# Kernel optimization log

Hardware: AMD Instinct MI355X
Metric: run time of the kernel (lower is better)

Reference implementation:

```python
import jax, jax.numpy as jnp
import numpy as np

N_USERS = 100000
N_ITEMS = 50000
N_NODES = N_USERS + N_ITEMS
D = 64
N_LAYERS = 3
POP_BINS = 10
NNZ = 2000000
BATCH = 256
BIAS_SCALE = 1.0


def setup_inputs() -> dict:
    key = jax.random.key(0)
    ks = jax.random.split(key, 16)
    std = 0.01
    inp = {
        "user_emb": jax.random.normal(ks[0], (N_USERS, D), jnp.float32) * std,
        "item_emb": jax.random.normal(ks[1], (N_ITEMS, D), jnp.float32) * std,
        "user_bias": jnp.zeros((N_USERS, 1), jnp.float32),
        "item_bias": jnp.zeros((N_ITEMS, 1), jnp.float32),
        "pop_emb": jax.random.normal(ks[2], (POP_BINS, D), jnp.float32) * std,
        "uW1": jax.random.normal(ks[3], (D, D), jnp.float32) / np.sqrt(D),
        "ub1": jnp.zeros((D,), jnp.float32),
        "uW2": jax.random.normal(ks[4], (D, D), jnp.float32) / np.sqrt(D),
        "ub2": jnp.zeros((D,), jnp.float32),
        "iW1": jax.random.normal(ks[5], (D, D), jnp.float32) / np.sqrt(D),
        "ib1": jnp.zeros((D,), jnp.float32),
        "iW2": jax.random.normal(ks[6], (D, D), jnp.float32) / np.sqrt(D),
        "ib2": jnp.zeros((D,), jnp.float32),
        "gW1": jax.random.normal(ks[7], (2 * D, D), jnp.float32) / np.sqrt(2 * D),
        "gb1": jnp.zeros((D,), jnp.float32),
        "gW2": jax.random.normal(ks[8], (D, 1), jnp.float32) / np.sqrt(D),
        "gb2": jnp.zeros((1,), jnp.float32),
        "adj_vals": jax.random.uniform(ks[9], (NNZ,), jnp.float32),
        "adj_rows": jax.random.randint(ks[10], (NNZ,), 0, N_NODES, jnp.int32),
        "adj_cols": jax.random.randint(ks[11], (NNZ,), 0, N_NODES, jnp.int32),
        "item_pop_bins": jax.random.randint(ks[12], (N_ITEMS,), 0, POP_BINS, jnp.int32),
        "users": jax.random.randint(ks[13], (BATCH,), 0, N_USERS, jnp.int32),
    }
    return inp


def _spmm(vals, rows, cols, E):
    # sparse (N x N) @ E  via gather + segment-sum
    msgs = vals[:, None] * E[cols]          # [nnz, d]
    return jax.ops.segment_sum(msgs, rows, num_segments=N_NODES)


def _mlp2(x, W1, b1, W2, b2):
    return jax.nn.relu(x @ W1 + b1) @ W2 + b2


def reference(user_emb, item_emb, user_bias, item_bias, pop_emb,
              uW1, ub1, uW2, ub2, iW1, ib1, iW2, ib2,
              gW1, gb1, gW2, gb2,
              adj_vals, adj_rows, adj_cols, item_pop_bins, users):
    # ---- computer(): LightGCN propagation with uniform layer weights ----
    emb = jnp.concatenate([user_emb, item_emb], axis=0)   # [N, d]
    w = 1.0 / (N_LAYERS + 1)
    out = emb * w
    cur = emb
    for _ in range(N_LAYERS):
        cur = _spmm(adj_vals, adj_rows, adj_cols, cur)
        out = out + cur * w
    all_users, all_items = out[:N_USERS], out[N_USERS:]

    # ---- popularity-gated item fusion ----
    p_vec = pop_emb[item_pop_bins]                         # [n_items, d]
    gate_in = jnp.concatenate([all_items, p_vec], axis=-1)
    z = jax.nn.sigmoid(_mlp2(gate_in, gW1, gb1, gW2, gb2)) # [n_items, 1]
    items_fused = (1.0 - z) * all_items + z * p_vec

    # ---- two-tower scoring over all items ----
    U = _mlp2(all_users[users], uW1, ub1, uW2, ub2)        # [B, d]
    I = _mlp2(items_fused, iW1, ib1, iW2, ib2)             # [n_items, d]
    scores = U @ I.T                                        # [B, n_items]
    scores = scores + user_bias[users] * BIAS_SCALE + (item_bias.T) * BIAS_SCALE
    return scores
```

## Files before the change

### kernel.cpp

```cpp
#include <hip/hip_runtime.h>
#include <hip/hip_fp16.h>

#define N_USERS 100000
#define N_ITEMS 50000
#define N_NODES 150000
#define D 64
#define NNZ 2000000
#define BATCH 256
#define POP_BINS 10

#define BSH 9
#define NB2 293
#define CAP 8192
#define P1_EPB 2048
#define P1_BLOCKS 978

#define ST_P 130

__global__ __launch_bounds__(256) void k_prep(const float* __restrict__ ue,
                                              const float* __restrict__ ie,
                                              __half* __restrict__ Eh,
                                              const float* __restrict__ pop,
                                              const float* __restrict__ gW1,
                                              const float* __restrict__ iW1,
                                              float* __restrict__ hp,
                                              float* __restrict__ pp1) {
  int b = blockIdx.x;
  if (b == 9375) {
    for (int idx = threadIdx.x; idx < 2 * POP_BINS * 64; idx += 256) {
      int q = idx;
      bool second = q >= POP_BINS * 64;
      if (second) q -= POP_BINS * 64;
      int bb = q >> 6, o = q & 63;
      float s = 0.f;
      if (!second) {
        for (int k = 0; k < 64; k++) s += pop[bb * 64 + k] * gW1[(64 + k) * 64 + o];
        hp[q] = s;
      } else {
        for (int k = 0; k < 64; k++) s += pop[bb * 64 + k] * iW1[k * 64 + o];
        pp1[q] = s;
      }
    }
    return;
  }
  int t = b * 256 + threadIdx.x;
  size_t fo = (size_t)t * 4;
  const float* src = (fo < (size_t)N_USERS * 64) ? ue + fo
                                                 : ie + (fo - (size_t)N_USERS * 64);
  float4 v = *(const float4*)src;
  __half2* dst = (__half2*)(Eh + fo);
  dst[0] = __floats2half2_rn(v.x, v.y);
  dst[1] = __floats2half2_rn(v.z, v.w);
}

__global__ __launch_bounds__(256) void k_p1(const int* __restrict__ rows,
                                            const int* __restrict__ cols,
                                            const float* __restrict__ vals,
                                            int* __restrict__ bcur,
                                            uint2* __restrict__ gstage) {
  __shared__ int cnt[NB2];
  __shared__ int gbase[NB2];
  int t = threadIdx.x;
  for (int i = t; i < NB2; i += 256) cnt[i] = 0;
  __syncthreads();
  int base = blockIdx.x * P1_EPB;
  for (int i = 0; i < 8; i++) {
    int e = base + i * 256 + t;
    if (e < NNZ) atomicAdd(&cnt[rows[e] >> BSH], 1);
  }
  __syncthreads();
  for (int i = t; i < NB2; i += 256) {
    int c = cnt[i];
    gbase[i] = c ? atomicAdd(&bcur[i], c) : 0;
    cnt[i] = 0;
  }
  __syncthreads();
  for (int i = 0; i < 8; i++) {
    int e = base + i * 256 + t;
    if (e < NNZ) {
      int r = rows[e];
      int b = r >> BSH;
      int rank = atomicAdd(&cnt[b], 1);
      unsigned key = ((unsigned)(r & 511) << 18) | (unsigned)cols[e];
      gstage[(size_t)b * CAP + gbase[b] + rank] =
          make_uint2(key, __float_as_uint(vals[e]));
    }
  }
}

__global__ __launch_bounds__(512) void k_p2(const int* __restrict__ bcur,
                                            const uint2* __restrict__ gstage,
                                            uint2* __restrict__ epack,
                                            int* __restrict__ rowbeg,
                                            int* __restrict__ rowend,
                                            int* __restrict__ gcursor,
                                            const int* __restrict__ users,
                                            int* __restrict__ uflag,
                                            int* __restrict__ ulist,
                                            int* __restrict__ ucnt) {
  int b = blockIdx.x, t = threadIdx.x;
  if (b == NB2) {
    if (t < BATCH) {
      int u = users[t];
      int old = atomicOr(&uflag[u >> 5], 1 << (u & 31));
      if (!((old >> (u & 31)) & 1)) {
        int p = atomicAdd(ucnt, 1);
        ulist[p] = u;
      }
    }
    return;
  }
  __shared__ int cnt[512];
  __shared__ int off[512];
  __shared__ int s[512];
  __shared__ int gbs;
  __shared__ uint2 buf[CAP];
  int n = bcur[b];
  const uint2* gs = gstage + (size_t)b * CAP;
  if (t == 0) gbs = atomicAdd(gcursor, n);
  cnt[t] = 0;
  __syncthreads();
  for (int j = t; j < n; j += 512)
    atomicAdd(&cnt[gs[j].x >> 18], 1);
  __syncthreads();
  int v = cnt[t];
  s[t] = v;
  __syncthreads();
  for (int o = 1; o < 512; o <<= 1) {
    int x = (t >= o) ? s[t - o] : 0;
    __syncthreads();
    s[t] += x;
    __syncthreads();
  }
  int ex = s[t] - v;
  off[t] = ex;
  int base = gbs;
  int gr = (b << BSH) + t;
  if (gr < N_NODES) { rowbeg[gr] = base + ex; rowend[gr] = base + ex + v; }
  __syncthreads();
  for (int j = t; j < n; j += 512) {
    uint2 ed = gs[j];
    int lr = ed.x >> 18;
    int pos = atomicAdd(&off[lr], 1);
    buf[pos] = make_uint2(ed.x & 0x3FFFFu, ed.y);
  }
  __syncthreads();
  for (int j = t; j < n; j += 512) epack[base + j] = buf[j];
}

#define SPMM_QW_BODY(TBL)                                                     \
  float a0 = 0.f, a1 = 0.f, a2 = 0.f, a3 = 0.f;                               \
  int j = beg;                                                                \
  for (; j + 7 < end; j += 8) {                                               \
    uint2 ea = epack[j + q];                                                  \
    uint2 eb = epack[j + 4 + q];                                              \
    uint2 ra = *(const uint2*)(TBL + (size_t)ea.x * 64 + 4 * p);              \
    uint2 rb = *(const uint2*)(TBL + (size_t)eb.x * 64 + 4 * p);              \
    float va = __uint_as_float(ea.y), vb = __uint_as_float(eb.y);             \
    float2 la = __half22float2(*(const __half2*)&ra.x);                       \
    float2 ha = __half22float2(*(const __half2*)&ra.y);                       \
    float2 lb = __half22float2(*(const __half2*)&rb.x);                       \
    float2 hb = __half22float2(*(const __half2*)&rb.y);                       \
    a0 += va * la.x; a1 += va * la.y; a2 += va * ha.x; a3 += va * ha.y;       \
    a0 += vb * lb.x; a1 += vb * lb.y; a2 += vb * hb.x; a3 += vb * hb.y;       \
  }                                                                           \
  for (; j < end; j += 4) {                                                   \
    int jj = j + q;                                                           \
    int jc = (jj < end) ? jj : end - 1;                                       \
    uint2 e = epack[jc];                                                      \
    float v = (jj < end) ? __uint_as_float(e.y) : 0.f;                        \
    uint2 r = *(const uint2*)(TBL + (size_t)e.x * 64 + 4 * p);                \
    float2 lo = __half22float2(*(const __half2*)&r.x);                        \
    float2 hi = __half22float2(*(const __half2*)&r.y);                        \
    a0 += v * lo.x; a1 += v * lo.y; a2 += v * hi.x; a3 += v * hi.y;           \
  }                                                                           \
  a0 += __shfl_xor(a0, 16, 64); a0 += __shfl_xor(a0, 32, 64);                 \
  a1 += __shfl_xor(a1, 16, 64); a1 += __shfl_xor(a1, 32, 64);                 \
  a2 += __shfl_xor(a2, 16, 64); a2 += __shfl_xor(a2, 32, 64);                 \
  a3 += __shfl_xor(a3, 16, 64); a3 += __shfl_xor(a3, 32, 64);

__global__ __launch_bounds__(256) void k_spmm1(const int* __restrict__ rowbeg,
                                               const int* __restrict__ rowend,
                                               const uint2* __restrict__ epack,
                                               const float* __restrict__ ue,
                                               const float* __restrict__ ie,
                                               const __half* __restrict__ Eh0,
                                               const int* __restrict__ uflag,
                                               __half* __restrict__ EoutH,
                                               float* __restrict__ Oacc) {
  int wave = blockIdx.x * 4 + (threadIdx.x >> 6);
  int row = __builtin_amdgcn_readfirstlane(wave);
  if (row >= N_NODES) return;
  int lane = threadIdx.x & 63;
  int p = lane & 15, q = lane >> 4;
  int beg = rowbeg[row];
  int end = rowend[row];
  SPMM_QW_BODY(Eh0)
  if (q == 0) {
    __half2* eo = (__half2*)(EoutH + (size_t)row * 64 + 4 * p);
    eo[0] = __floats2half2_rn(a0, a1);
    eo[1] = __floats2half2_rn(a2, a3);
    bool need = (row >= N_USERS) || (((uflag[row >> 5] >> (row & 31)) & 1) != 0);
    if (need) {
      const float* srow = (row < N_USERS) ? ue + (size_t)row * 64
                                          : ie + (size_t)(row - N_USERS) * 64;
      float4 sv = *(const float4*)(srow + 4 * p);
      *(float4*)(Oacc + (size_t)row * 64 + 4 * p) =
          make_float4(0.25f * (sv.x + a0), 0.25f * (sv.y + a1),
                      0.25f * (sv.z + a2), 0.25f * (sv.w + a3));
    }
  }
}

__global__ __launch_bounds__(256) void k_spmm2h(const int* __restrict__ rowbeg,
                                                const int* __restrict__ rowend,
                                                const uint2* __restrict__ epack,
                                                const __half* __restrict__ Ein,
                                                const int* __restrict__ uflag,
                                                __half* __restrict__ EoutH,
                                                float* __restrict__ Oacc) {
  int wave = blockIdx.x * 4 + (threadIdx.x >> 6);
  int row = __builtin_amdgcn_readfirstlane(wave);
  if (row >= N_NODES) return;
  int lane = threadIdx.x & 63;
  int p = lane & 15, q = lane >> 4;
  int beg = rowbeg[row];
  int end = rowend[row];
  SPMM_QW_BODY(Ein)
  if (q == 0) {
    __half2* eo = (__half2*)(EoutH + (size_t)row * 64 + 4 * p);
    eo[0] = __floats2half2_rn(a0, a1);
    eo[1] = __floats2half2_rn(a2, a3);
    if (row >= N_USERS || (((uflag[row >> 5] >> (row & 31)) & 1) != 0)) {
      float4* op = (float4*)(Oacc + (size_t)row * 64 + 4 * p);
      float4 cur = *op;
      *op = make_float4(cur.x + 0.25f * a0, cur.y + 0.25f * a1,
                        cur.z + 0.25f * a2, cur.w + 0.25f * a3);
    }
  }
}

__global__ __launch_bounds__(256) void k_spmm3h(const int* __restrict__ rowbeg,
                                                const int* __restrict__ rowend,
                                                const uint2* __restrict__ epack,
                                                const __half* __restrict__ Ein,
                                                const int* __restrict__ ulist,
                                                const int* __restrict__ ucnt,
                                                float* __restrict__ Oacc) {
  int w = blockIdx.x * 4 + (threadIdx.x >> 6);
  int row;
  if (w < N_ITEMS) {
    row = N_USERS + w;
  } else {
    int k = w - N_ITEMS;
    if (k >= ucnt[0]) return;
    row = ulist[k];
  }
  row = __builtin_amdgcn_readfirstlane(row);
  int lane = threadIdx.x & 63;
  int p = lane & 15, q = lane >> 4;
  int beg = rowbeg[row];
  int end = rowend[row];
  SPMM_QW_BODY(Ein)
  if (q == 0) {
    float4* op = (float4*)(Oacc + (size_t)row * 64 + 4 * p);
    float4 cur = *op;
    *op = make_float4(cur.x + 0.25f * a0, cur.y + 0.25f * a1,
                      cur.z + 0.25f * a2, cur.w + 0.25f * a3);
  }
}

__global__ __launch_bounds__(256) void k_user(const float* __restrict__ Oacc,
                                              const int* __restrict__ users,
                                              const float* __restrict__ ubias,
                                              const float* __restrict__ uW1,
                                              const float* __restrict__ ub1,
                                              const float* __restrict__ uW2,
                                              const float* __restrict__ ub2,
                                              float* __restrict__ Ut) {
  int ub = blockIdx.x * 4 + (threadIdx.x >> 6);
  int lane = threadIdx.x & 63;
  int u = users[ub];
  float x = Oacc[(size_t)u * 64 + lane];
  float h = ub1[lane];
#pragma unroll
  for (int k = 0; k < 64; k++)
    h = fmaf(__shfl(x, k, 64), uW1[k * 64 + lane], h);
  h = h > 0.f ? h : 0.f;
  float o = ub2[lane];
#pragma unroll
  for (int k = 0; k < 64; k++)
    o = fmaf(__shfl(h, k, 64), uW2[k * 64 + lane], o);
  Ut[lane * 256 + ub] = o;
  if (lane == 0) Ut[64 * 256 + ub] = ubias[u];
}

__global__ __launch_bounds__(256) void k_gemm12(const float* __restrict__ Oacc,
                                                const float* __restrict__ gW1,
                                                const float* __restrict__ iW1,
                                                const int* __restrict__ bins,
                                                const float* __restrict__ hp,
                                                const float* __restrict__ pp1,
                                                const float* __restrict__ gb1,
                                                const float* __restrict__ gW2,
                                                const float* __restrict__ gb2,
                                                const float* __restrict__ ib1,
                                                const float* __restrict__ iW2,
                                                const float* __restrict__ ib2,
                                                float* __restrict__ I) {
  __shared__ float Is[64 * ST_P];
  __shared__ float Bs[64 * 128];
  __shared__ float zp[128][9];
  __shared__ float zs[128];
  int tid = threadIdx.x;
  int i0 = blockIdx.x * 128;
  {
    int c4 = tid & 15, r0 = tid >> 4;
#pragma unroll
    for (int s = 0; s < 8; s++) {
      int r = r0 + s * 16;
      int it = i0 + r;
      float4 v = make_float4(0.f, 0.f, 0.f, 0.f);
      if (it < N_ITEMS) v = *(const float4*)(Oacc + (size_t)(N_USERS + it) * 64 + c4 * 4);
      Is[(c4 * 4 + 0) * ST_P + r] = v.x;
      Is[(c4 * 4 + 1) * ST_P + r] = v.y;
      Is[(c4 * 4 + 2) * ST_P + r] = v.z;
      Is[(c4 * 4 + 3) * ST_P + r] = v.w;
    }
  }
  for (int idx = tid; idx < 64 * 128; idx += 256) {
    int k = idx >> 7, o = idx & 127;
    Bs[idx] = (o < 64) ? gW1[k * 64 + o] : iW1[k * 64 + (o - 64)];
  }
  __syncthreads();
  int tx = tid & 15, ty = tid >> 4;
  float acc[8][8];
#pragma unroll
  for (int a = 0; a < 8; a++)
#pragma unroll
    for (int b = 0; b < 8; b++) acc[a][b] = 0.f;
  {
    const float* ip = Is + tx * 8;
    const float* wp = Bs + ty * 8;
#pragma unroll 2
    for (int k = 0; k < 64; k++) {
      float4 iv0 = *(const float4*)(ip + k * ST_P);
      float4 iv1 = *(const float4*)(ip + k * ST_P + 4);
      float4 wv0 = *(const float4*)(wp + k * 128);
      float4 wv1 = *(const float4*)(wp + k * 128 + 4);
      float iv[8] = {iv0.x, iv0.y, iv0.z, iv0.w, iv1.x, iv1.y, iv1.z, iv1.w};
      float wv[8] = {wv0.x, wv0.y, wv0.z, wv0.w, wv1.x, wv1.y, wv1.z, wv1.w};
#pragma unroll
      for (int a = 0; a < 8; a++)
#pragma unroll
        for (int b = 0; b < 8; b++) acc[a][b] += iv[a] * wv[b];
    }
  }
  int ibase = i0 + tx * 8;
  if (ty < 8) {
    int o0 = ty * 8;
#pragma unroll
    for (int a = 0; a < 8; a++) {
      int it = ibase + a;
      float p = 0.f;
      if (it < N_ITEMS) {
        int bin = bins[it];
        const float* hpr = hp + bin * 64 + o0;
#pragma unroll
        for (int b = 0; b < 8; b++) {
          float g = acc[a][b] + hpr[b] + gb1[o0 + b];
          g = g > 0.f ? g : 0.f;
          p += g * gW2[o0 + b];
        }
      }
      zp[tx * 8 + a][ty] = p;
    }
  }
  __syncthreads();
  if (tid < 128) {
    float s = gb2[0];
#pragma unroll
    for (int k = 0; k < 8; k++) s += zp[tid][k];
    zs[tid] = 1.f / (1.f + expf(-s));
  }
  __syncthreads();
  if (ty >= 8) {
    int o0 = (ty - 8) * 8;
#pragma unroll
    for (int a = 0; a < 8; a++) {
      int it = ibase + a;
      int item = tx * 8 + a;
      float z = zs[item];
      int bin = (it < N_ITEMS) ? bins[it] : 0;
      const float* ppr = pp1 + bin * 64 + o0;
#pragma unroll
      for (int b = 0; b < 8; b++) {
        float v = (1.f - z) * acc[a][b] + z * ppr[b] + ib1[o0 + b];
        Is[(o0 + b) * ST_P + item] = v > 0.f ? v : 0.f;
      }
    }
  }
  for (int idx = tid; idx < 64 * 64; idx += 256) Bs[idx] = iW2[idx];
  __syncthreads();
  float acc2[8][4];
#pragma unroll
  for (int a = 0; a < 8; a++)
#pragma unroll
    for (int b = 0; b < 4; b++) acc2[a][b] = 0.f;
  {
    const float* ip = Is + tx * 8;
    const float* wp = Bs + ty * 4;
#pragma unroll 2
    for (int k = 0; k < 64; k++) {
      float4 iv0 = *(const float4*)(ip + k * ST_P);
      float4 iv1 = *(const float4*)(ip + k * ST_P + 4);
      float4 wv = *(const float4*)(wp + k * 64);
      float iv[8] = {iv0.x, iv0.y, iv0.z, iv0.w, iv1.x, iv1.y, iv1.z, iv1.w};
      float wvv[4] = {wv.x, wv.y, wv.z, wv.w};
#pragma unroll
      for (int a = 0; a < 8; a++)
#pragma unroll
        for (int b = 0; b < 4; b++) acc2[a][b] += iv[a] * wvv[b];
    }
  }
  int oc = ty * 4;
  float b0 = ib2[oc], b1 = ib2[oc + 1], b2 = ib2[oc + 2], b3 = ib2[oc + 3];
#pragma unroll
  for (int a = 0; a < 8; a++) {
    int it = ibase + a;
    if (it < N_ITEMS) {
      float4 s0 = make_float4(acc2[a][0] + b0, acc2[a][1] + b1,
                              acc2[a][2] + b2, acc2[a][3] + b3);
      *(float4*)(I + (size_t)it * 64 + oc) = s0;
    }
  }
}

__global__ __launch_bounds__(256) void k_scores(const float* __restrict__ I,
                                                const float* __restrict__ Ut,
                                                const float* __restrict__ item_bias,
                                                float* __restrict__ out) {
  __shared__ float Is[64 * ST_P];
  __shared__ float Us[64 * 128];
  int tid = threadIdx.x;
  int i0 = blockIdx.x * 128;
  {
    int c4 = tid & 15, r0 = tid >> 4;
#pragma unroll
    for (int s = 0; s < 8; s++) {
      int r = r0 + s * 16;
      int it = i0 + r;
      float4 v = make_float4(0.f, 0.f, 0.f, 0.f);
      if (it < N_ITEMS) v = *(const float4*)(I + (size_t)it * 64 + c4 * 4);
      Is[(c4 * 4 + 0) * ST_P + r] = v.x;
      Is[(c4 * 4 + 1) * ST_P + r] = v.y;
      Is[(c4 * 4 + 2) * ST_P + r] = v.z;
      Is[(c4 * 4 + 3) * ST_P + r] = v.w;
    }
  }
  int tx = tid & 15;
  int ty = tid >> 4;
  int ibase = i0 + tx * 8;
  float ib[8];
#pragma unroll
  for (int a = 0; a < 8; a++)
    ib[a] = (ibase + a < N_ITEMS) ? item_bias[ibase + a] : 0.f;
  for (int uh = 0; uh < 2; uh++) {
    int ubase = uh * 128;
    if (uh) __syncthreads();
    {
      int u4 = tid & 31, k0 = tid >> 5;
#pragma unroll
      for (int s = 0; s < 8; s++) {
        int k = k0 + s * 8;
        float4 v = *(const float4*)(Ut + k * 256 + ubase + u4 * 4);
        *(float4*)(Us + k * 128 + u4 * 4) = v;
      }
    }
    __syncthreads();
    float acc[8][8];
#pragma unroll
    for (int a = 0; a < 8; a++)
#pragma unroll
      for (int b = 0; b < 8; b++) acc[a][b] = 0.f;
    const float* ip = Is + tx * 8;
    const float* up = Us + ty * 8;
#pragma unroll 2
    for (int k = 0; k < 64; k++) {
      float4 iv0 = *(const float4*)(ip + k * ST_P);
      float4 iv1 = *(const float4*)(ip + k * ST_P + 4);
      float4 uv0 = *(const float4*)(up + k * 128);
      float4 uv1 = *(const float4*)(up + k * 128 + 4);
      float iv[8] = {iv0.x, iv0.y, iv0.z, iv0.w, iv1.x, iv1.y, iv1.z, iv1.w};
      float uv[8] = {uv0.x, uv0.y, uv0.z, uv0.w, uv1.x, uv1.y, uv1.z, uv1.w};
#pragma unroll
      for (int a = 0; a < 8; a++)
#pragma unroll
        for (int b = 0; b < 8; b++) acc[a][b] += iv[a] * uv[b];
    }
#pragma unroll
    for (int bb = 0; bb < 8; bb++) {
      int bu = ubase + ty * 8 + bb;
      float ubias = Ut[64 * 256 + bu];
      float* orow = out + (size_t)bu * N_ITEMS + ibase;
      if (ibase + 7 < N_ITEMS) {
        float4 s0 = make_float4(acc[0][bb] + ubias + ib[0], acc[1][bb] + ubias + ib[1],
                                acc[2][bb] + ubias + ib[2], acc[3][bb] + ubias + ib[3]);
        float4 s1 = make_float4(acc[4][bb] + ubias + ib[4], acc[5][bb] + ubias + ib[5],
                                acc[6][bb] + ubias + ib[6], acc[7][bb] + ubias + ib[7]);
        *(float4*)orow = s0;
        *(float4*)(orow + 4) = s1;
      } else {
#pragma unroll
        for (int a = 0; a < 8; a++)
          if (ibase + a < N_ITEMS) orow[a] = acc[a][bb] + ubias + ib[a];
      }
    }
  }
}

extern "C" void kernel_launch(void* const* d_in, const int* in_sizes, int n_in,
                              void* d_out, int out_size, void* d_ws, size_t ws_size,
                              hipStream_t stream) {
  const float* user_emb  = (const float*)d_in[0];
  const float* item_emb  = (const float*)d_in[1];
  const float* user_bias = (const float*)d_in[2];
  const float* item_bias = (const float*)d_in[3];
  const float* pop_emb   = (const float*)d_in[4];
  const float* uW1 = (const float*)d_in[5];
  const float* ub1 = (const float*)d_in[6];
  const float* uW2 = (const float*)d_in[7];
  const float* ub2 = (const float*)d_in[8];
  const float* iW1 = (const float*)d_in[9];
  const float* ib1 = (const float*)d_in[10];
  const float* iW2 = (const float*)d_in[11];
  const float* ib2 = (const float*)d_in[12];
  const float* gW1 = (const float*)d_in[13];
  const float* gb1 = (const float*)d_in[14];
  const float* gW2 = (const float*)d_in[15];
  const float* gb2 = (const float*)d_in[16];
  const float* adj_vals = (const float*)d_in[17];
  const int* adj_rows = (const int*)d_in[18];
  const int* adj_cols = (const int*)d_in[19];
  const int* bins  = (const int*)d_in[20];
  const int* users = (const int*)d_in[21];
  float* out = (float*)d_out;

  float* ws = (float*)d_ws;
  float* Oacc = ws;
  float* bufA = ws + 9600000;
  float* bufB = ws + 19200000;
  uint2* epack = (uint2*)(ws + 28800000);
  int* rowbeg = (int*)(ws + 32800000);
  int* rowend = (int*)(ws + 32950000);
  int* uflag   = (int*)(ws + 33100000);
  int* ucnt    = (int*)(ws + 33103125);
  int* bcur    = (int*)(ws + 33103126);
  int* gcursor = (int*)(ws + 33103419);
  int* ulist   = (int*)(ws + 33103420);
  float* Ut   = ws + 33104000;
  float* hp   = ws + 33121000;
  float* pp1  = ws + 33122000;
  uint2* gstage = (uint2*)bufB;
  __half* Eh0 = (__half*)bufA;
  __half* E1h = (__half*)(bufA + 4800000);
  __half* E2h = (__half*)bufB;
  float* I  = bufB;

  hipMemsetAsync(uflag, 0, 3680 * sizeof(int), stream);
  k_prep<<<9376, 256, 0, stream>>>(user_emb, item_emb, Eh0, pop_emb, gW1, iW1, hp, pp1);
  k_p1<<<P1_BLOCKS, 256, 0, stream>>>(adj_rows, adj_cols, adj_vals, bcur, gstage);
  k_p2<<<NB2 + 1, 512, 0, stream>>>(bcur, gstage, epack, rowbeg, rowend, gcursor,
                                    users, uflag, ulist, ucnt);

  k_spmm1<<<37500, 256, 0, stream>>>(rowbeg, rowend, epack, user_emb, item_emb,
                                     Eh0, uflag, E1h, Oacc);
  k_spmm2h<<<37500, 256, 0, stream>>>(rowbeg, rowend, epack, E1h, uflag, E2h, Oacc);
  k_spmm3h<<<12564, 256, 0, stream>>>(rowbeg, rowend, epack, E2h, ulist, ucnt, Oacc);

  k_user<<<64, 256, 0, stream>>>(Oacc, users, user_bias, uW1, ub1, uW2, ub2, Ut);
  k_gemm12<<<391, 256, 0, stream>>>(Oacc, gW1, iW1, bins, hp, pp1, gb1, gW2, gb2,
                                    ib1, iW2, ib2, I);
  k_scores<<<391, 256, 0, stream>>>(I, Ut, item_bias, out);
}
```

Measured before the change: 486.2 us.

## Replace two-pass bucketed CSR build with histogram, wave-scan claim, and atomic scatter

Replaces the bucketed two-phase COO-to-CSR conversion (shared-memory staging into 293 buckets, then a per-bucket local sort) with three simple kernels. A global per-row atomic histogram is followed by a wavefront-scan kernel that claims contiguous ranges via a global cursor, and then an atomic-cursor scatter writes edges directly into epack. This removes the staging buffer round trip and the per-bucket shared-memory sort, at the cost of 2M global atomics on random rows twice. Row order in memory is no longer row-sorted globally, and edge order within a row becomes nondeterministic.

```diff
diff --git a/kernel.cpp b/kernel.cpp
--- a/kernel.cpp
+++ b/kernel.cpp
@@ -9,11 +9,9 @@
 #define BATCH 256
 #define POP_BINS 10
 
-#define BSH 9
-#define NB2 293
-#define CAP 8192
-#define P1_EPB 2048
-#define P1_BLOCKS 978
+#define H_EPB 2048
+#define H_BLOCKS 978
+#define CLAIM_BLOCKS 587
 
 #define ST_P 130
 
@@ -53,53 +51,26 @@
   dst[1] = __floats2half2_rn(v.z, v.w);
 }
 
-__global__ __launch_bounds__(256) void k_p1(const int* __restrict__ rows,
-                                            const int* __restrict__ cols,
-                                            const float* __restrict__ vals,
-                                            int* __restrict__ bcur,
-                                            uint2* __restrict__ gstage) {
-  __shared__ int cnt[NB2];
-  __shared__ int gbase[NB2];
+__global__ __launch_bounds__(256) void k_hist(const int* __restrict__ rows,
+                                              int* __restrict__ rtmp) {
+  int base = blockIdx.x * H_EPB;
   int t = threadIdx.x;
-  for (int i = t; i < NB2; i += 256) cnt[i] = 0;
-  __syncthreads();
-  int base = blockIdx.x * P1_EPB;
   for (int i = 0; i < 8; i++) {
     int e = base + i * 256 + t;
-    if (e < NNZ) atomicAdd(&cnt[rows[e] >> BSH], 1);
-  }
-  __syncthreads();
-  for (int i = t; i < NB2; i += 256) {
-    int c = cnt[i];
-    gbase[i] = c ? atomicAdd(&bcur[i], c) : 0;
-    cnt[i] = 0;
-  }
-  __syncthreads();
-  for (int i = 0; i < 8; i++) {
-    int e = base + i * 256 + t;
-    if (e < NNZ) {
-      int r = rows[e];
-      int b = r >> BSH;
-      int rank = atomicAdd(&cnt[b], 1);
-      unsigned key = ((unsigned)(r & 511) << 18) | (unsigned)cols[e];
-      gstage[(size_t)b * CAP + gbase[b] + rank] =
-          make_uint2(key, __float_as_uint(vals[e]));
-    }
-  }
-}
-
-__global__ __launch_bounds__(512) void k_p2(const int* __restrict__ bcur,
-                                            const uint2* __restrict__ gstage,
-                                            uint2* __restrict__ epack,
-                                            int* __restrict__ rowbeg,
-                                            int* __restrict__ rowend,
-                                            int* __restrict__ gcursor,
-                                            const int* __restrict__ users,
-                                            int* __restrict__ uflag,
-                                            int* __restrict__ ulist,
-                                            int* __restrict__ ucnt) {
-  int b = blockIdx.x, t = threadIdx.x;
-  if (b == NB2) {
+    if (e < NNZ) atomicAdd(&rtmp[rows[e]], 1);
+  }
+}
+
+__global__ __launch_bounds__(256) void k_claim(int* __restrict__ rtmp,
+                                               int* __restrict__ rowbeg,
+                                               int* __restrict__ rowend,
+                                               int* __restrict__ gcursor,
+                                               const int* __restrict__ users,
+                                               int* __restrict__ uflag,
+                                               int* __restrict__ ulist,
+                                               int* __restrict__ ucnt) {
+  int t = threadIdx.x;
+  if (blockIdx.x == CLAIM_BLOCKS - 1) {
     if (t < BATCH) {
       int u = users[t];
       int old = atomicOr(&uflag[u >> 5], 1 << (u & 31));
@@ -110,42 +81,42 @@
     }
     return;
   }
-  __shared__ int cnt[512];
-  __shared__ int off[512];
-  __shared__ int s[512];
-  __shared__ int gbs;
-  __shared__ uint2 buf[CAP];
-  int n = bcur[b];
-  const uint2* gs = gstage + (size_t)b * CAP;
-  if (t == 0) gbs = atomicAdd(gcursor, n);
-  cnt[t] = 0;
-  __syncthreads();
-  for (int j = t; j < n; j += 512)
-    atomicAdd(&cnt[gs[j].x >> 18], 1);
-  __syncthreads();
-  int v = cnt[t];
-  s[t] = v;
-  __syncthreads();
-  for (int o = 1; o < 512; o <<= 1) {
-    int x = (t >= o) ? s[t - o] : 0;
-    __syncthreads();
-    s[t] += x;
-    __syncthreads();
-  }
-  int ex = s[t] - v;
-  off[t] = ex;
-  int base = gbs;
-  int gr = (b << BSH) + t;
-  if (gr < N_NODES) { rowbeg[gr] = base + ex; rowend[gr] = base + ex + v; }
-  __syncthreads();
-  for (int j = t; j < n; j += 512) {
-    uint2 ed = gs[j];
-    int lr = ed.x >> 18;
-    int pos = atomicAdd(&off[lr], 1);
-    buf[pos] = make_uint2(ed.x & 0x3FFFFu, ed.y);
-  }
-  __syncthreads();
-  for (int j = t; j < n; j += 512) epack[base + j] = buf[j];
+  int lane = t & 63;
+  int row = blockIdx.x * 256 + (t >> 6) * 64 + lane;
+  int c = (row < N_NODES) ? rtmp[row] : 0;
+  int incl = c;
+#pragma unroll
+  for (int off = 1; off < 64; off <<= 1) {
+    int x = __shfl_up(incl, off, 64);
+    if (lane >= off) incl += x;
+  }
+  int total = __shfl(incl, 63, 64);
+  int basev = 0;
+  if (lane == 63) basev = atomicAdd(gcursor, total);
+  int base = __shfl(basev, 63, 64);
+  int beg = base + incl - c;
+  if (row < N_NODES) {
+    rowbeg[row] = beg;
+    rowend[row] = beg + c;
+    rtmp[row] = beg;
+  }
+}
+
+__global__ __launch_bounds__(256) void k_scatter(const int* __restrict__ rows,
+                                                 const int* __restrict__ cols,
+                                                 const float* __restrict__ vals,
+                                                 int* __restrict__ rtmp,
+                                                 uint2* __restrict__ epack) {
+  int base = blockIdx.x * H_EPB;
+  int t = threadIdx.x;
+  for (int i = 0; i < 8; i++) {
+    int e = base + i * 256 + t;
+    if (e < NNZ) {
+      int r = rows[e];
+      int pos = atomicAdd(&rtmp[r], 1);
+      epack[pos] = make_uint2((unsigned)cols[e], __float_as_uint(vals[e]));
+    }
+  }
 }
 
 #define SPMM_QW_BODY(TBL)                                                     \
@@ -555,23 +526,24 @@
   int* rowend = (int*)(ws + 32950000);
   int* uflag   = (int*)(ws + 33100000);
   int* ucnt    = (int*)(ws + 33103125);
-  int* bcur    = (int*)(ws + 33103126);
-  int* gcursor = (int*)(ws + 33103419);
-  int* ulist   = (int*)(ws + 33103420);
+  int* gcursor = (int*)(ws + 33103126);
+  int* ulist   = (int*)(ws + 33103127);
   float* Ut   = ws + 33104000;
   float* hp   = ws + 33121000;
   float* pp1  = ws + 33122000;
-  uint2* gstage = (uint2*)bufB;
+  int* rtmp = (int*)bufB;
   __half* Eh0 = (__half*)bufA;
   __half* E1h = (__half*)(bufA + 4800000);
   __half* E2h = (__half*)bufB;
   float* I  = bufB;
 
-  hipMemsetAsync(uflag, 0, 3680 * sizeof(int), stream);
+  hipMemsetAsync(uflag, 0, 3400 * sizeof(int), stream);
+  hipMemsetAsync(rtmp, 0, N_NODES * sizeof(int), stream);
   k_prep<<<9376, 256, 0, stream>>>(user_emb, item_emb, Eh0, pop_emb, gW1, iW1, hp, pp1);
-  k_p1<<<P1_BLOCKS, 256, 0, stream>>>(adj_rows, adj_cols, adj_vals, bcur, gstage);
-  k_p2<<<NB2 + 1, 512, 0, stream>>>(bcur, gstage, epack, rowbeg, rowend, gcursor,
-                                    users, uflag, ulist, ucnt);
+  k_hist<<<H_BLOCKS, 256, 0, stream>>>(adj_rows, rtmp);
+  k_claim<<<CLAIM_BLOCKS, 256, 0, stream>>>(rtmp, rowbeg, rowend, gcursor,
+                                            users, uflag, ulist, ucnt);
+  k_scatter<<<H_BLOCKS, 256, 0, stream>>>(adj_rows, adj_cols, adj_vals, rtmp, epack);
 
   k_spmm1<<<37500, 256, 0, stream>>>(rowbeg, rowend, epack, user_emb, item_emb,
                                      Eh0, uflag, E1h, Oacc);
```

Result: slower. 665.5 us (+36.9%).
